# Optimization experiments

Hardware: AMD Instinct MI355X
Metric: run time of the kernel (lower is better)

Reference implementation:

```python
import jax, jax.numpy as jnp
import numpy as np

TANH_CONST = 1.5  # tanh_constant in __init__
EPS = 1e-9


def setup_inputs() -> dict:
    key = jax.random.key(0)
    ks = jax.random.split(key, 6)
    B, H, NOPS, T = 8192, 100, 5, 512
    return {
        "x0": jax.random.uniform(ks[0], (B, H), dtype=jnp.float32),          # g_emb-style uniform start input
        "W_x": jax.random.normal(ks[1], (H, 4 * H), dtype=jnp.float32) * 0.1,  # LSTMCell kernel (no bias)
        "W_h": jax.random.normal(ks[2], (H, 4 * H), dtype=jnp.float32) * 0.1,  # LSTMCell recurrent kernel
        "W_ops": jax.random.normal(ks[3], (H, NOPS), dtype=jnp.float32) * 0.1, # dense_ops (no bias)
        "emb": jax.random.normal(ks[4], (NOPS + 1, H), dtype=jnp.float32),     # Embedding(num_ops+1, lstm_size)
        "u": jax.random.uniform(ks[5], (T, B, NOPS), dtype=jnp.float32),       # uniform noise -> Gumbel-max sampling
    }


def reference(x0, W_x, W_h, W_ops, emb, u):
    # Gumbel noise for categorical sampling (equiv. in distribution to tf.random.categorical)
    g = -jnp.log(-jnp.log(u + EPS) + EPS)  # [T, B, num_ops]
    B, H = x0.shape

    def step(carry, g_t):
        h, c, x = carry
        # Keras LSTMCell, use_bias=False: gate order (i, f, c, o)
        z = x @ W_x + h @ W_h                      # [B, 4H]
        zi, zf, zc, zo = jnp.split(z, 4, axis=-1)
        c_new = jax.nn.sigmoid(zf) * c + jax.nn.sigmoid(zi) * jnp.tanh(zc)
        h_new = jax.nn.sigmoid(zo) * jnp.tanh(c_new)
        logits = TANH_CONST * jnp.tanh(h_new @ W_ops)  # tanh_constant * tanh(dense_ops(h))
        op = jnp.argmax(logits + g_t, axis=-1)         # [B] sampled op ids
        logp = jax.nn.log_softmax(logits, axis=-1)
        cur = -jnp.take_along_axis(logp, op[:, None], axis=-1)[:, 0]  # sparse xent vs sampled label
        ent = jax.lax.stop_gradient(cur * jnp.exp(-cur))
        x_new = emb[op]                                # next-step input = embedding(op_id)
        return (h_new, c_new, x_new), (cur, ent, op)

    h0 = jnp.zeros((B, H), x0.dtype)
    c0 = jnp.zeros((B, H), x0.dtype)
    _, (curs, ents, ops) = jax.lax.scan(step, (h0, c0, x0), g)
    log_prob = curs.sum(0)   # [B] accumulated self.log_prob
    entropy = ents.sum(0)    # [B] accumulated self.entropy
    return log_prob, entropy, ops
```

## Files before the change

### kernel.cpp

```cpp
#include <hip/hip_runtime.h>
#include <cstdint>
#include <cstddef>

typedef __attribute__((ext_vector_type(8))) short short8;
typedef __attribute__((ext_vector_type(4))) short bfx4;
typedef __attribute__((ext_vector_type(4))) float f32x4;

#define HH     100
#define G4     400
#define NCOL   416
#define NTIL   26
#define KTN    3
#define KRES   96
#define BTOT   8192
#define TST    512
#define ROWS   32
#define NBLK   256
#define BLOCK  512
#define ZW     420
#define TANHC  1.5f
#define EPSF   1e-9f

__device__ unsigned short d_Bhi[NTIL*KTN*64*8];
__device__ unsigned short d_Blo[NTIL*KTN*64*8];
__device__ float d_Ep2[6*G4];
__device__ float d_WresG[NCOL*4];
__device__ float d_Z0[(size_t)BTOT*G4];

static __device__ __forceinline__ unsigned short bf16hi(float f){
  unsigned u = __float_as_uint(f);
  return (unsigned short)((u + 0x7FFFu + ((u>>16)&1u)) >> 16);
}
static __device__ __forceinline__ float bf16f(unsigned short s){
  return __uint_as_float(((unsigned)s)<<16);
}
static __device__ __forceinline__ float frcp(float x){ return __builtin_amdgcn_rcpf(x); }
static __device__ __forceinline__ float sigf(float x){ return frcp(1.0f + __expf(-x)); }
static __device__ __forceinline__ float tanh_f(float x){ return 1.0f - 2.0f*frcp(__expf(2.0f*x) + 1.0f); }


__global__ void setup_bpack(const float* __restrict__ Wh, const float* __restrict__ Wops){
  int idx = blockIdx.x*blockDim.x + threadIdx.x;
  if (idx >= NTIL*KTN*64) return;
  int tile = idx/(KTN*64), rem = idx - tile*(KTN*64), kt = rem>>6, ln = rem&63;
  int n = tile*16 + (ln & 15);
  #pragma unroll
  for (int i = 0; i < 8; ++i){
    int k = kt*32 + (ln>>4)*8 + i;
    float w = 0.f;
    if (n < G4)          w = Wh[k*G4 + n];
    else if (n < G4+5)   w = Wops[k*5 + (n - G4)];
    unsigned short hi = bf16hi(w);
    unsigned short lo = bf16hi(w - bf16f(hi));
    d_Bhi[idx*8+i] = hi;
    d_Blo[idx*8+i] = lo;
  }
}

__global__ void setup_misc(const float* __restrict__ emb, const float* __restrict__ Wx,
                           const float* __restrict__ Wh, const float* __restrict__ Wops){
  int idx = blockIdx.x*blockDim.x + threadIdx.x;
  if (idx < 6*G4){
    int e = idx/G4, r2 = idx - e*G4, je = r2>>2, g = r2&3;
    float s = 0.f;
    for (int k = 0; k < HH; ++k) s = fmaf(emb[e*HH+k], Wx[k*G4 + g*HH + je], s);
    d_Ep2[idx] = s;
  } else if (idx < 6*G4 + NCOL*4){
    int i = idx - 6*G4, n = i>>2, q = i&3;
    float w = 0.f;
    if (n < G4)        w = Wh[(KRES+q)*G4 + n];
    else if (n < G4+5) w = Wops[(KRES+q)*5 + (n - G4)];
    d_WresG[i] = w;
  }
}

__global__ __launch_bounds__(256) void setup_z0(const float* __restrict__ x0,
                                                const float* __restrict__ Wx){
  __shared__ float xs[64*101];
  const int bb = blockIdx.x * 64;
  for (int i = threadIdx.x; i < 64*HH; i += 256){
    int r = i/HH, k = i - r*HH;
    xs[r*101 + k] = x0[(size_t)(bb + r)*HH + k];
  }
  __syncthreads();
  const int bl = threadIdx.x & 63;
  for (int ng = threadIdx.x >> 6; ng < HH; ng += 4){
    f32x4 a = {0.f,0.f,0.f,0.f};
    for (int k = 0; k < HH; ++k){
      f32x4 w = *(const f32x4*)&Wx[k*G4 + ng*4];
      a += w * xs[bl*101 + k];
    }
    *(f32x4*)&d_Z0[(size_t)(bb + bl)*G4 + ng*4] = a;
  }
}


__global__ __launch_bounds__(BLOCK, 2) void rnn_main(
    const float* __restrict__ u, float* __restrict__ out)
{
  __shared__ __align__(16) float z_lds[ROWS*ZW];
  __shared__ __align__(16) unsigned short fhi[2*KTN*64*8];
  __shared__ __align__(16) unsigned short flo[2*KTN*64*8];
  __shared__ __align__(16) float h_res[4*ROWS];
  __shared__ __align__(16) float Ep2_l[6*G4];
  __shared__ __align__(16) float Wres_l[NCOL*4];
  __shared__ __align__(16) float samp[5*36];
  __shared__ __align__(16) float gn_lds[ROWS*5];
  __shared__ int op_lds[ROWS];

  const int tid  = threadIdx.x;
  const int wave = tid >> 6;
  const int lane = tid & 63;
  const int cn   = lane & 15;
  const int q4   = lane >> 4;
  const int row0 = blockIdx.x * ROWS;
  const int rE   = tid & 31;

  for (int i = tid; i < 6*G4;   i += BLOCK) Ep2_l[i]  = d_Ep2[i];
  for (int i = tid; i < NCOL*4; i += BLOCK) Wres_l[i] = d_WresG[i];

  const int tb  = (wave==0) ? 23 : (wave < 6) ? 3*(wave-1) : 15 + 4*(wave-6);
  const int ntl = (wave >= 6) ? 4 : 3;
  short8 bh[4][KTN], bl[4][KTN];
  {
    const short8* bph = (const short8*)d_Bhi;
    const short8* bpl = (const short8*)d_Blo;
    #pragma unroll
    for (int tl = 0; tl < 4; ++tl) if (tl < ntl)
      #pragma unroll
      for (int kt = 0; kt < KTN; ++kt){
        int fi = ((tb+tl)*KTN + kt)*64 + lane;
        bh[tl][kt] = bph[fi];
        bl[tl][kt] = bpl[fi];
      }
  }

  float cs1[4] = {0.f,0.f,0.f,0.f};
  float cs2[4] = {0.f,0.f,0.f,0.f};
  float lp_acc = 0.f, ent_acc = 0.f;

  for (int t = 0; t <= TST; ++t){
    float upr[5];
    if (t < TST && tid >= 416 && tid < 448){
      const float* up = u + ((size_t)t*BTOT + row0 + (tid - 416))*5;
      #pragma unroll
      for (int o = 0; o < 5; ++o) upr[o] = up[o];
    }

    if (t == 0){
      for (int i = tid; i < ROWS*HH; i += BLOCK){
        int r = i/HH, c4 = i - r*HH;
        *(f32x4*)&z_lds[r*ZW + c4*4] =
          *(const f32x4*)&d_Z0[(size_t)(row0 + r)*G4 + c4*4];
      }
    } else {
      #pragma unroll
      for (int mt = 0; mt < 2; ++mt){
        short8 ah[KTN], al[KTN];
        #pragma unroll
        for (int kt = 0; kt < KTN; ++kt){
          ah[kt] = *(const short8*)&fhi[((mt*KTN + kt)*64 + lane)*8];
          al[kt] = *(const short8*)&flo[((mt*KTN + kt)*64 + lane)*8];
        }
        f32x4 hq[4];
        #pragma unroll
        for (int q = 0; q < 4; ++q)
          hq[q] = *(const f32x4*)&h_res[q*ROWS + mt*16 + q4*4];
        #pragma unroll
        for (int tl = 0; tl < 4; ++tl) if (tl < ntl){
          const int n = (tb+tl)*16 + cn;
          f32x4 acc = {0.f,0.f,0.f,0.f};
          #pragma unroll
          for (int kt = 0; kt < KTN; ++kt){
            acc = __builtin_amdgcn_mfma_f32_16x16x32_bf16(ah[kt], bh[tl][kt], acc, 0,0,0);
            acc = __builtin_amdgcn_mfma_f32_16x16x32_bf16(al[kt], bh[tl][kt], acc, 0,0,0);
            acc = __builtin_amdgcn_mfma_f32_16x16x32_bf16(ah[kt], bl[tl][kt], acc, 0,0,0);
            acc = __builtin_amdgcn_mfma_f32_16x16x32_bf16(al[kt], bl[tl][kt], acc, 0,0,0);
          }
          f32x4 wr = *(const f32x4*)&Wres_l[n*4];
          #pragma unroll
          for (int q = 0; q < 4; ++q) acc += hq[q] * wr[q];
          const int rowb = mt*16 + q4*4;
          #pragma unroll
          for (int i = 0; i < 4; ++i)
            z_lds[(rowb + i)*ZW + n] = acc[i];
          if (wave == 0 && tl == 2 && cn < 5)
            *(f32x4*)&samp[cn*36 + mt*16 + q4*4] = acc;
        }
      }
      if (wave == 0 && lane < 32){
        int r = lane;
        float l[5];
        #pragma unroll
        for (int o = 0; o < 5; ++o) l[o] = TANHC * tanh_f(samp[o*36 + r]);
        int op = 0; float best = -1e30f;
        #pragma unroll
        for (int o = 0; o < 5; ++o){
          float v = l[o] + gn_lds[r*5 + o];
          if (v > best){ best = v; op = o; }
        }
        float mx = fmaxf(fmaxf(fmaxf(l[0],l[1]), fmaxf(l[2],l[3])), l[4]);
        float se = 0.f;
        #pragma unroll
        for (int o = 0; o < 5; ++o) se += __expf(l[o] - mx);
        float lse = mx + __logf(se);
        float cur = lse - l[op];
        lp_acc  += cur;
        ent_acc += cur * __expf(-cur);
        op_lds[r] = op;
        out[2*BTOT + (size_t)(t-1)*BTOT + row0 + r] = (float)op;
      }
    }
    if (t == TST) break;
    __syncthreads();

    {
      const int jg = tid >> 5;
      f32x4 zg[4];
      #pragma unroll
      for (int g = 0; g < 4; ++g)
        zg[g] = *(const f32x4*)&z_lds[rE*ZW + g*HH + jg*4];
      if (t > 0){
        const int op = op_lds[rE];
        #pragma unroll
        for (int i = 0; i < 4; ++i){
          f32x4 e4 = *(const f32x4*)&Ep2_l[op*G4 + (jg*4 + i)*4];
          zg[0][i] += e4.x; zg[1][i] += e4.y; zg[2][i] += e4.z; zg[3][i] += e4.w;
        }
      }
      float hv[4];
      #pragma unroll
      for (int i = 0; i < 4; ++i){
        float cn_ = sigf(zg[1][i])*cs1[i] + sigf(zg[0][i])*tanh_f(zg[2][i]);
        cs1[i] = cn_;
        hv[i] = sigf(zg[3][i])*tanh_f(cn_);
      }
      bfx4 h4, l4;
      #pragma unroll
      for (int i = 0; i < 4; ++i){
        unsigned short hi = bf16hi(hv[i]);
        h4[i] = (short)hi;
        l4[i] = (short)bf16hi(hv[i] - bf16f(hi));
      }
      const int kt   = jg >> 3;
      const int lf   = (rE & 15) | (((jg >> 1) & 3) << 4);
      const int mt   = rE >> 4;
      const int j0   = (jg & 1) * 4;
      const int base = ((mt*KTN + kt)*64 + lf)*8 + j0;
      *(bfx4*)&fhi[base] = h4;
      *(bfx4*)&flo[base] = l4;
    }
    if (tid < 256 || tid >= 480){
      const int jg = (tid < 256) ? (16 + (tid >> 5)) : 24;
      const int c0 = jg*4;
      f32x4 zg[4];
      #pragma unroll
      for (int g = 0; g < 4; ++g)
        zg[g] = *(const f32x4*)&z_lds[rE*ZW + g*HH + c0];
      if (t > 0){
        const int op = op_lds[rE];
        #pragma unroll
        for (int i = 0; i < 4; ++i){
          f32x4 e4 = *(const f32x4*)&Ep2_l[op*G4 + (c0 + i)*4];
          zg[0][i] += e4.x; zg[1][i] += e4.y; zg[2][i] += e4.z; zg[3][i] += e4.w;
        }
      }
      float hv[4];
      #pragma unroll
      for (int i = 0; i < 4; ++i){
        float cn_ = sigf(zg[1][i])*cs2[i] + sigf(zg[0][i])*tanh_f(zg[2][i]);
        cs2[i] = cn_;
        hv[i] = sigf(zg[3][i])*tanh_f(cn_);
      }
      if (tid < 256){
        bfx4 h4, l4;
        #pragma unroll
        for (int i = 0; i < 4; ++i){
          unsigned short hi = bf16hi(hv[i]);
          h4[i] = (short)hi;
          l4[i] = (short)bf16hi(hv[i] - bf16f(hi));
        }
        const int kt   = jg >> 3;
        const int lf   = (rE & 15) | (((jg >> 1) & 3) << 4);
        const int mt   = rE >> 4;
        const int j0   = (jg & 1) * 4;
        const int base = ((mt*KTN + kt)*64 + lf)*8 + j0;
        *(bfx4*)&fhi[base] = h4;
        *(bfx4*)&flo[base] = l4;
      } else {
        #pragma unroll
        for (int i = 0; i < 4; ++i) h_res[i*ROWS + rE] = hv[i];
      }
    } else if (tid >= 416 && tid < 448){
      int r = tid - 416;
      #pragma unroll
      for (int o = 0; o < 5; ++o)
        gn_lds[r*5 + o] = -__logf(-__logf(upr[o] + EPSF) + EPSF);
    }
    __syncthreads();
  }

  if (wave == 0 && lane < 32){
    out[row0 + lane]        = lp_acc;
    out[BTOT + row0 + lane] = ent_acc;
  }
}

extern "C" void kernel_launch(void* const* d_in, const int* in_sizes, int n_in,
                              void* d_out, int out_size, void* d_ws, size_t ws_size,
                              hipStream_t stream) {
  const float* x0   = (const float*)d_in[0];
  const float* Wx   = (const float*)d_in[1];
  const float* Wh   = (const float*)d_in[2];
  const float* Wops = (const float*)d_in[3];
  const float* emb  = (const float*)d_in[4];
  const float* u    = (const float*)d_in[5];
  (void)d_ws; (void)ws_size; (void)in_sizes; (void)n_in;

  setup_bpack<<<(NTIL*KTN*64 + 255)/256, 256, 0, stream>>>(Wh, Wops);
  setup_misc<<<(6*G4 + NCOL*4 + 255)/256, 256, 0, stream>>>(emb, Wx, Wh, Wops);
  setup_z0<<<BTOT/64, 256, 0, stream>>>(x0, Wx);
  rnn_main<<<NBLK, BLOCK, 0, stream>>>(u, (float*)d_out);
}
```

Measured before the change: 2.081 ms.

## Drop lo*lo MFMA term and compute op logits via transposed MFMA in registers

After: 1.986 ms. -4.6%, faster.

```diff
diff --git a/kernel.cpp b/kernel.cpp
--- a/kernel.cpp
+++ b/kernel.cpp
@@ -104,7 +104,6 @@
   __shared__ __align__(16) float h_res[4*ROWS];
   __shared__ __align__(16) float Ep2_l[6*G4];
   __shared__ __align__(16) float Wres_l[NCOL*4];
-  __shared__ __align__(16) float samp[5*36];
   __shared__ __align__(16) float gn_lds[ROWS*5];
   __shared__ int op_lds[ROWS];
 
@@ -121,6 +120,7 @@
 
   const int tb  = (wave==0) ? 23 : (wave < 6) ? 3*(wave-1) : 15 + 4*(wave-6);
   const int ntl = (wave >= 6) ? 4 : 3;
+  const int ngt = (wave == 0) ? 2 : ntl;
   short8 bh[4][KTN], bl[4][KTN];
   {
     const short8* bph = (const short8*)d_Bhi;
@@ -154,6 +154,7 @@
           *(const f32x4*)&d_Z0[(size_t)(row0 + r)*G4 + c4*4];
       }
     } else {
+      f32x4 accT[2];
       #pragma unroll
       for (int mt = 0; mt < 2; ++mt){
         short8 ah[KTN], al[KTN];
@@ -167,7 +168,7 @@
         for (int q = 0; q < 4; ++q)
           hq[q] = *(const f32x4*)&h_res[q*ROWS + mt*16 + q4*4];
         #pragma unroll
-        for (int tl = 0; tl < 4; ++tl) if (tl < ntl){
+        for (int tl = 0; tl < 4; ++tl) if (tl < ngt){
           const int n = (tb+tl)*16 + cn;
           f32x4 acc = {0.f,0.f,0.f,0.f};
           #pragma unroll
@@ -175,7 +176,6 @@
             acc = __builtin_amdgcn_mfma_f32_16x16x32_bf16(ah[kt], bh[tl][kt], acc, 0,0,0);
             acc = __builtin_amdgcn_mfma_f32_16x16x32_bf16(al[kt], bh[tl][kt], acc, 0,0,0);
             acc = __builtin_amdgcn_mfma_f32_16x16x32_bf16(ah[kt], bl[tl][kt], acc, 0,0,0);
-            acc = __builtin_amdgcn_mfma_f32_16x16x32_bf16(al[kt], bl[tl][kt], acc, 0,0,0);
           }
           f32x4 wr = *(const f32x4*)&Wres_l[n*4];
           #pragma unroll
@@ -184,36 +184,71 @@
           #pragma unroll
           for (int i = 0; i < 4; ++i)
             z_lds[(rowb + i)*ZW + n] = acc[i];
-          if (wave == 0 && tl == 2 && cn < 5)
-            *(f32x4*)&samp[cn*36 + mt*16 + q4*4] = acc;
-        }
-      }
-      if (wave == 0 && lane < 32){
-        int r = lane;
-        float l[5];
-        #pragma unroll
-        for (int o = 0; o < 5; ++o) l[o] = TANHC * tanh_f(samp[o*36 + r]);
-        int op = 0; float best = -1e30f;
-        #pragma unroll
-        for (int o = 0; o < 5; ++o){
-          float v = l[o] + gn_lds[r*5 + o];
-          if (v > best){ best = v; op = o; }
-        }
-        float mx = fmaxf(fmaxf(fmaxf(l[0],l[1]), fmaxf(l[2],l[3])), l[4]);
-        float se = 0.f;
-        #pragma unroll
-        for (int o = 0; o < 5; ++o) se += __expf(l[o] - mx);
-        float lse = mx + __logf(se);
-        float cur = lse - l[op];
-        lp_acc  += cur;
-        ent_acc += cur * __expf(-cur);
-        op_lds[r] = op;
-        out[2*BTOT + (size_t)(t-1)*BTOT + row0 + r] = (float)op;
+        }
+        if (wave == 0){
+          f32x4 a = {0.f,0.f,0.f,0.f};
+          #pragma unroll
+          for (int kt = 0; kt < KTN; ++kt){
+            a = __builtin_amdgcn_mfma_f32_16x16x32_bf16(bh[2][kt], ah[kt], a, 0,0,0);
+            a = __builtin_amdgcn_mfma_f32_16x16x32_bf16(bh[2][kt], al[kt], a, 0,0,0);
+            a = __builtin_amdgcn_mfma_f32_16x16x32_bf16(bl[2][kt], ah[kt], a, 0,0,0);
+          }
+          accT[mt] = a;
+        }
+      }
+      if (wave == 0){
+        #pragma unroll
+        for (int mt = 0; mt < 2; ++mt){
+          const int rr = mt*16 + cn;
+          float h0 = h_res[0*ROWS + rr], h1 = h_res[1*ROWS + rr];
+          float h2 = h_res[2*ROWS + rr], h3 = h_res[3*ROWS + rr];
+          #pragma unroll
+          for (int i = 0; i < 4; ++i){
+            f32x4 wr = *(const f32x4*)&Wres_l[(G4 + q4*4 + i)*4];
+            accT[mt][i] += h0*wr.x + h1*wr.y + h2*wr.z + h3*wr.w;
+          }
+        }
+        float o4lo = __shfl_down(accT[0][0], 16);
+        float t1o0 = __shfl_up(accT[1][0], 16);
+        float t1o1 = __shfl_up(accT[1][1], 16);
+        float t1o2 = __shfl_up(accT[1][2], 16);
+        float t1o3 = __shfl_up(accT[1][3], 16);
+        if (lane < 32){
+          const int r = lane;
+          float raw[5];
+          if (lane < 16){
+            raw[0] = accT[0][0]; raw[1] = accT[0][1];
+            raw[2] = accT[0][2]; raw[3] = accT[0][3]; raw[4] = o4lo;
+          } else {
+            raw[0] = t1o0; raw[1] = t1o1; raw[2] = t1o2; raw[3] = t1o3;
+            raw[4] = accT[1][0];
+          }
+          float l[5];
+          #pragma unroll
+          for (int o = 0; o < 5; ++o) l[o] = TANHC * tanh_f(raw[o]);
+          int op = 0; float best = -1e30f;
+          #pragma unroll
+          for (int o = 0; o < 5; ++o){
+            float v = l[o] + gn_lds[r*5 + o];
+            if (v > best){ best = v; op = o; }
+          }
+          float mx = fmaxf(fmaxf(fmaxf(l[0],l[1]), fmaxf(l[2],l[3])), l[4]);
+          float se = 0.f;
+          #pragma unroll
+          for (int o = 0; o < 5; ++o) se += __expf(l[o] - mx);
+          float lse = mx + __logf(se);
+          float cur = lse - l[op];
+          lp_acc  += cur;
+          ent_acc += cur * __expf(-cur);
+          op_lds[r] = op;
+          out[2*BTOT + (size_t)(t-1)*BTOT + row0 + r] = (float)op;
+        }
       }
     }
     if (t == TST) break;
     __syncthreads();
 
+    const int opv = (t > 0) ? op_lds[rE] : 0;
     {
       const int jg = tid >> 5;
       f32x4 zg[4];
@@ -221,10 +256,9 @@
       for (int g = 0; g < 4; ++g)
         zg[g] = *(const f32x4*)&z_lds[rE*ZW + g*HH + jg*4];
       if (t > 0){
-        const int op = op_lds[rE];
         #pragma unroll
         for (int i = 0; i < 4; ++i){
-          f32x4 e4 = *(const f32x4*)&Ep2_l[op*G4 + (jg*4 + i)*4];
+          f32x4 e4 = *(const f32x4*)&Ep2_l[opv*G4 + (jg*4 + i)*4];
           zg[0][i] += e4.x; zg[1][i] += e4.y; zg[2][i] += e4.z; zg[3][i] += e4.w;
         }
       }
@@ -258,10 +292,9 @@
       for (int g = 0; g < 4; ++g)
         zg[g] = *(const f32x4*)&z_lds[rE*ZW + g*HH + c0];
       if (t > 0){
-        const int op = op_lds[rE];
         #pragma unroll
         for (int i = 0; i < 4; ++i){
-          f32x4 e4 = *(const f32x4*)&Ep2_l[op*G4 + (c0 + i)*4];
+          f32x4 e4 = *(const f32x4*)&Ep2_l[opv*G4 + (c0 + i)*4];
           zg[0][i] += e4.x; zg[1][i] += e4.y; zg[2][i] += e4.z; zg[3][i] += e4.w;
         }
       }
```

## Shrink blocks to 16 rows with 4 waves and rebalance MFMA tile assignment

Applied to the files above, without the earlier changes.

Result: no change. 2.100 ms (+0.9%).

```diff
diff --git a/kernel.cpp b/kernel.cpp
--- a/kernel.cpp
+++ b/kernel.cpp
@@ -14,9 +14,9 @@
 #define KRES   96
 #define BTOT   8192
 #define TST    512
-#define ROWS   32
-#define NBLK   256
-#define BLOCK  512
+#define GR     16
+#define NBLK   512
+#define BLOCK  256
 #define ZW     420
 #define TANHC  1.5f
 #define EPSF   1e-9f
@@ -98,38 +98,49 @@
 __global__ __launch_bounds__(BLOCK, 2) void rnn_main(
     const float* __restrict__ u, float* __restrict__ out)
 {
-  __shared__ __align__(16) float z_lds[ROWS*ZW];
-  __shared__ __align__(16) unsigned short fhi[2*KTN*64*8];
-  __shared__ __align__(16) unsigned short flo[2*KTN*64*8];
-  __shared__ __align__(16) float h_res[4*ROWS];
+  __shared__ __align__(16) float z_lds[GR*ZW];
+  __shared__ __align__(16) unsigned short fhi[KTN*64*8];
+  __shared__ __align__(16) unsigned short flo[KTN*64*8];
+  __shared__ __align__(16) float h_res[4*GR];
   __shared__ __align__(16) float Ep2_l[6*G4];
   __shared__ __align__(16) float Wres_l[NCOL*4];
-  __shared__ __align__(16) float samp[5*36];
-  __shared__ __align__(16) float gn_lds[ROWS*5];
-  __shared__ int op_lds[ROWS];
+  __shared__ __align__(16) float gn_lds[GR*5];
+  __shared__ int op_lds[GR];
 
   const int tid  = threadIdx.x;
   const int wave = tid >> 6;
   const int lane = tid & 63;
   const int cn   = lane & 15;
   const int q4   = lane >> 4;
-  const int row0 = blockIdx.x * ROWS;
-  const int rE   = tid & 31;
+  const int row0 = blockIdx.x * GR;
+  const int rE   = tid & 15;
+
+  if (blockIdx.x & 256){
+    __builtin_amdgcn_s_sleep(24);
+    __builtin_amdgcn_s_sleep(24);
+  }
 
   for (int i = tid; i < 6*G4;   i += BLOCK) Ep2_l[i]  = d_Ep2[i];
   for (int i = tid; i < NCOL*4; i += BLOCK) Wres_l[i] = d_WresG[i];
 
-  const int tb  = (wave==0) ? 23 : (wave < 6) ? 3*(wave-1) : 15 + 4*(wave-6);
-  const int ntl = (wave >= 6) ? 4 : 3;
-  short8 bh[4][KTN], bl[4][KTN];
+  const int ntl = (wave==0 || wave==2) ? 7 : 6;
+  const int ngt = (wave==3) ? 5 : ntl;
+  int tids[7];
+  #pragma unroll
+  for (int tl = 0; tl < 7; ++tl)
+    tids[tl] = (wave==0) ? (tl<6 ? tl      : 24)
+             : (wave==1) ? (6+tl)
+             : (wave==2) ? (tl<6 ? 12+tl   : 23)
+             :             (tl<5 ? 18+tl   : 25);
+  short8 bh[7][KTN], bl[7][KTN];
   {
     const short8* bph = (const short8*)d_Bhi;
     const short8* bpl = (const short8*)d_Blo;
     #pragma unroll
-    for (int tl = 0; tl < 4; ++tl) if (tl < ntl)
+    for (int tl = 0; tl < 7; ++tl) if (tl < ntl)
       #pragma unroll
       for (int kt = 0; kt < KTN; ++kt){
-        int fi = ((tb+tl)*KTN + kt)*64 + lane;
+        int fi = (tids[tl]*KTN + kt)*64 + lane;
         bh[tl][kt] = bph[fi];
         bl[tl][kt] = bpl[fi];
       }
@@ -141,90 +152,104 @@
 
   for (int t = 0; t <= TST; ++t){
     float upr[5];
-    if (t < TST && tid >= 416 && tid < 448){
-      const float* up = u + ((size_t)t*BTOT + row0 + (tid - 416))*5;
+    if (t < TST && tid >= 208 && tid < 224){
+      const float* up = u + ((size_t)t*BTOT + row0 + (tid - 208))*5;
       #pragma unroll
       for (int o = 0; o < 5; ++o) upr[o] = up[o];
     }
 
     if (t == 0){
-      for (int i = tid; i < ROWS*HH; i += BLOCK){
+      for (int i = tid; i < GR*HH; i += BLOCK){
         int r = i/HH, c4 = i - r*HH;
         *(f32x4*)&z_lds[r*ZW + c4*4] =
           *(const f32x4*)&d_Z0[(size_t)(row0 + r)*G4 + c4*4];
       }
     } else {
-      #pragma unroll
-      for (int mt = 0; mt < 2; ++mt){
-        short8 ah[KTN], al[KTN];
+      short8 ah[KTN], al[KTN];
+      #pragma unroll
+      for (int kt = 0; kt < KTN; ++kt){
+        ah[kt] = *(const short8*)&fhi[(kt*64 + lane)*8];
+        al[kt] = *(const short8*)&flo[(kt*64 + lane)*8];
+      }
+      f32x4 hq[4];
+      #pragma unroll
+      for (int q = 0; q < 4; ++q)
+        hq[q] = *(const f32x4*)&h_res[q*GR + q4*4];
+      #pragma unroll
+      for (int tl = 0; tl < 7; ++tl) if (tl < ngt){
+        const int n = tids[tl]*16 + cn;
+        f32x4 acc = {0.f,0.f,0.f,0.f};
         #pragma unroll
         for (int kt = 0; kt < KTN; ++kt){
-          ah[kt] = *(const short8*)&fhi[((mt*KTN + kt)*64 + lane)*8];
-          al[kt] = *(const short8*)&flo[((mt*KTN + kt)*64 + lane)*8];
-        }
-        f32x4 hq[4];
-        #pragma unroll
-        for (int q = 0; q < 4; ++q)
-          hq[q] = *(const f32x4*)&h_res[q*ROWS + mt*16 + q4*4];
-        #pragma unroll
-        for (int tl = 0; tl < 4; ++tl) if (tl < ntl){
-          const int n = (tb+tl)*16 + cn;
-          f32x4 acc = {0.f,0.f,0.f,0.f};
+          acc = __builtin_amdgcn_mfma_f32_16x16x32_bf16(ah[kt], bh[tl][kt], acc, 0,0,0);
+          acc = __builtin_amdgcn_mfma_f32_16x16x32_bf16(al[kt], bh[tl][kt], acc, 0,0,0);
+          acc = __builtin_amdgcn_mfma_f32_16x16x32_bf16(ah[kt], bl[tl][kt], acc, 0,0,0);
+        }
+        f32x4 wr = *(const f32x4*)&Wres_l[n*4];
+        #pragma unroll
+        for (int q = 0; q < 4; ++q) acc += hq[q] * wr[q];
+        const int rowb = q4*4;
+        #pragma unroll
+        for (int i = 0; i < 4; ++i)
+          z_lds[(rowb + i)*ZW + n] = acc[i];
+      }
+      if (wave == 3){
+        f32x4 accT = {0.f,0.f,0.f,0.f};
+        #pragma unroll
+        for (int kt = 0; kt < KTN; ++kt){
+          accT = __builtin_amdgcn_mfma_f32_16x16x32_bf16(bh[5][kt], ah[kt], accT, 0,0,0);
+          accT = __builtin_amdgcn_mfma_f32_16x16x32_bf16(bh[5][kt], al[kt], accT, 0,0,0);
+          accT = __builtin_amdgcn_mfma_f32_16x16x32_bf16(bl[5][kt], ah[kt], accT, 0,0,0);
+        }
+        {
+          float h0 = h_res[0*GR + cn], h1 = h_res[1*GR + cn];
+          float h2 = h_res[2*GR + cn], h3 = h_res[3*GR + cn];
           #pragma unroll
-          for (int kt = 0; kt < KTN; ++kt){
-            acc = __builtin_amdgcn_mfma_f32_16x16x32_bf16(ah[kt], bh[tl][kt], acc, 0,0,0);
-            acc = __builtin_amdgcn_mfma_f32_16x16x32_bf16(al[kt], bh[tl][kt], acc, 0,0,0);
-            acc = __builtin_amdgcn_mfma_f32_16x16x32_bf16(ah[kt], bl[tl][kt], acc, 0,0,0);
-            acc = __builtin_amdgcn_mfma_f32_16x16x32_bf16(al[kt], bl[tl][kt], acc, 0,0,0);
+          for (int i = 0; i < 4; ++i){
+            f32x4 wr = *(const f32x4*)&Wres_l[(G4 + q4*4 + i)*4];
+            accT[i] += h0*wr.x + h1*wr.y + h2*wr.z + h3*wr.w;
           }
-          f32x4 wr = *(const f32x4*)&Wres_l[n*4];
+        }
+        float o4lo = __shfl_down(accT[0], 16);
+        if (lane < 16){
+          const int r = lane;
+          float raw[5] = {accT[0], accT[1], accT[2], accT[3], o4lo};
+          float l[5];
           #pragma unroll
-          for (int q = 0; q < 4; ++q) acc += hq[q] * wr[q];
-          const int rowb = mt*16 + q4*4;
+          for (int o = 0; o < 5; ++o) l[o] = TANHC * tanh_f(raw[o]);
+          int op = 0; float best = -1e30f;
           #pragma unroll
-          for (int i = 0; i < 4; ++i)
-            z_lds[(rowb + i)*ZW + n] = acc[i];
-          if (wave == 0 && tl == 2 && cn < 5)
-            *(f32x4*)&samp[cn*36 + mt*16 + q4*4] = acc;
-        }
-      }
-      if (wave == 0 && lane < 32){
-        int r = lane;
-        float l[5];
-        #pragma unroll
-        for (int o = 0; o < 5; ++o) l[o] = TANHC * tanh_f(samp[o*36 + r]);
-        int op = 0; float best = -1e30f;
-        #pragma unroll
-        for (int o = 0; o < 5; ++o){
-          float v = l[o] + gn_lds[r*5 + o];
-          if (v > best){ best = v; op = o; }
-        }
-        float mx = fmaxf(fmaxf(fmaxf(l[0],l[1]), fmaxf(l[2],l[3])), l[4]);
-        float se = 0.f;
-        #pragma unroll
-        for (int o = 0; o < 5; ++o) se += __expf(l[o] - mx);
-        float lse = mx + __logf(se);
-        float cur = lse - l[op];
-        lp_acc  += cur;
-        ent_acc += cur * __expf(-cur);
-        op_lds[r] = op;
-        out[2*BTOT + (size_t)(t-1)*BTOT + row0 + r] = (float)op;
+          for (int o = 0; o < 5; ++o){
+            float v = l[o] + gn_lds[r*5 + o];
+            if (v > best){ best = v; op = o; }
+          }
+          float mx = fmaxf(fmaxf(fmaxf(l[0],l[1]), fmaxf(l[2],l[3])), l[4]);
+          float se = 0.f;
+          #pragma unroll
+          for (int o = 0; o < 5; ++o) se += __expf(l[o] - mx);
+          float lse = mx + __logf(se);
+          float cur = lse - l[op];
+          lp_acc  += cur;
+          ent_acc += cur * __expf(-cur);
+          op_lds[r] = op;
+          out[2*BTOT + (size_t)(t-1)*BTOT + row0 + r] = (float)op;
+        }
       }
     }
     if (t == TST) break;
     __syncthreads();
 
+    const int opv = (t > 0) ? op_lds[rE] : 0;
     {
-      const int jg = tid >> 5;
+      const int jg = tid >> 4;
       f32x4 zg[4];
       #pragma unroll
       for (int g = 0; g < 4; ++g)
         zg[g] = *(const f32x4*)&z_lds[rE*ZW + g*HH + jg*4];
       if (t > 0){
-        const int op = op_lds[rE];
         #pragma unroll
         for (int i = 0; i < 4; ++i){
-          f32x4 e4 = *(const f32x4*)&Ep2_l[op*G4 + (jg*4 + i)*4];
+          f32x4 e4 = *(const f32x4*)&Ep2_l[opv*G4 + (jg*4 + i)*4];
           zg[0][i] += e4.x; zg[1][i] += e4.y; zg[2][i] += e4.z; zg[3][i] += e4.w;
         }
       }
@@ -243,25 +268,23 @@
         l4[i] = (short)bf16hi(hv[i] - bf16f(hi));
       }
       const int kt   = jg >> 3;
-      const int lf   = (rE & 15) | (((jg >> 1) & 3) << 4);
-      const int mt   = rE >> 4;
+      const int lf   = rE | (((jg >> 1) & 3) << 4);
       const int j0   = (jg & 1) * 4;
-      const int base = ((mt*KTN + kt)*64 + lf)*8 + j0;
+      const int base = (kt*64 + lf)*8 + j0;
       *(bfx4*)&fhi[base] = h4;
       *(bfx4*)&flo[base] = l4;
     }
-    if (tid < 256 || tid >= 480){
-      const int jg = (tid < 256) ? (16 + (tid >> 5)) : 24;
+    if (tid >= 64 && tid < 208){
+      const int jg = 24 - ((tid - 64) >> 4);
       const int c0 = jg*4;
       f32x4 zg[4];
       #pragma unroll
       for (int g = 0; g < 4; ++g)
         zg[g] = *(const f32x4*)&z_lds[rE*ZW + g*HH + c0];
       if (t > 0){
-        const int op = op_lds[rE];
         #pragma unroll
         for (int i = 0; i < 4; ++i){
-          f32x4 e4 = *(const f32x4*)&Ep2_l[op*G4 + (c0 + i)*4];
+          f32x4 e4 = *(const f32x4*)&Ep2_l[opv*G4 + (c0 + i)*4];
           zg[0][i] += e4.x; zg[1][i] += e4.y; zg[2][i] += e4.z; zg[3][i] += e4.w;
         }
       }
@@ -272,7 +295,7 @@
         cs2[i] = cn_;
         hv[i] = sigf(zg[3][i])*tanh_f(cn_);
       }
-      if (tid < 256){
+      if (jg < 24){
         bfx4 h4, l4;
         #pragma unroll
         for (int i = 0; i < 4; ++i){
@@ -281,18 +304,17 @@
           l4[i] = (short)bf16hi(hv[i] - bf16f(hi));
         }
         const int kt   = jg >> 3;
-        const int lf   = (rE & 15) | (((jg >> 1) & 3) << 4);
-        const int mt   = rE >> 4;
+        const int lf   = rE | (((jg >> 1) & 3) << 4);
         const int j0   = (jg & 1) * 4;
-        const int base = ((mt*KTN + kt)*64 + lf)*8 + j0;
+        const int base = (kt*64 + lf)*8 + j0;
         *(bfx4*)&fhi[base] = h4;
         *(bfx4*)&flo[base] = l4;
       } else {
         #pragma unroll
-        for (int i = 0; i < 4; ++i) h_res[i*ROWS + rE] = hv[i];
-      }
-    } else if (tid >= 416 && tid < 448){
-      int r = tid - 416;
+        for (int i = 0; i < 4; ++i) h_res[i*GR + rE] = hv[i];
+      }
+    } else if (tid >= 208 && tid < 224){
+      int r = tid - 208;
       #pragma unroll
       for (int o = 0; o < 5; ++o)
         gn_lds[r*5 + o] = -__logf(-__logf(upr[o] + EPSF) + EPSF);
@@ -300,7 +322,7 @@
     __syncthreads();
   }
 
-  if (wave == 0 && lane < 32){
+  if (wave == 3 && lane < 16){
     out[row0 + lane]        = lp_acc;
     out[BTOT + row0 + lane] = ent_acc;
   }
```
